# Kernel tuning notes

Hardware: AMD Instinct MI355X
Metric: run time of the kernel (lower is better)

## Reference

```python
import jax, jax.numpy as jnp
import numpy as np

OUT_H, OUT_W = 512, 512
BATCH, CHANNELS = 64, 3


def setup_inputs() -> dict:
    key = jax.random.key(0)
    k1, k2 = jax.random.split(key)
    U = jax.random.normal(k1, (BATCH, OUT_H, OUT_W, CHANNELS), dtype=jnp.float32)
    theta = jax.random.normal(k2, (BATCH, 1), dtype=jnp.float32)
    return {"U": U, "theta": theta}


def reference(U, theta):
    B = U.shape[0]
    H, W = OUT_H, OUT_W
    # normalized sampling grid [H*W, 3] with homogeneous coordinate
    gx, gy = jnp.meshgrid(jnp.linspace(-1.0, 1.0, W), jnp.linspace(-1.0, 1.0, H))
    grid = jnp.stack([gx, gy, jnp.ones_like(gx)], axis=-1).reshape(H * W, 3)
    # rotation-only affine matrix [B, 2, 3]
    cos_t, sin_t, z = jnp.cos(theta), jnp.sin(theta), jnp.zeros_like(theta)
    rot = jnp.concatenate([cos_t, -sin_t, z, sin_t, cos_t, z], axis=1).reshape(B, 2, 3)
    # transformed source coords [B, H*W, 2]
    T_g = jnp.einsum('bij,nj->bni', rot, grid)
    x = (T_g[..., 0] + 1.0) * (W - 1) / 2.0
    y = (T_g[..., 1] + 1.0) * (H - 1) / 2.0
    x0f = jnp.floor(x).astype(jnp.int32)
    y0f = jnp.floor(y).astype(jnp.int32)
    x0 = jnp.clip(x0f, 0, W - 1)
    x1 = jnp.clip(x0f + 1, 0, W - 1)
    y0 = jnp.clip(y0f, 0, H - 1)
    y1 = jnp.clip(y0f + 1, 0, H - 1)
    # 4-corner gathers, batched: [B, H*W, C]
    gather = jax.vmap(lambda u, yy, xx: u[yy, xx])
    Ia = gather(U, y0, x0)
    Ib = gather(U, y1, x0)
    Ic = gather(U, y0, x1)
    Id = gather(U, y1, x1)
    x0_f, x1_f = x0.astype(jnp.float32), x1.astype(jnp.float32)
    y0_f, y1_f = y0.astype(jnp.float32), y1.astype(jnp.float32)
    wa = (x1_f - x) * (y1_f - y)
    wb = (x1_f - x) * (y - y0_f)
    wc = (x - x0_f) * (y1_f - y)
    wd = (x - x0_f) * (y - y0_f)
    out = (wa[..., None] * Ia + wb[..., None] * Ib
           + wc[..., None] * Ic + wd[..., None] * Id)
    return out.reshape(B, H, W, -1)
```

## Files before the change

kernel.cpp:

```cpp
#include <hip/hip_runtime.h>
#include <hip/hip_fp16.h>

#define OUT_H 512
#define OUT_W 512
#define BATCH 64
#define CHANS 3

#define WROWS 48
#define WPX   48
#define RSTRIDE 98
#define LSZ 4704
#define IDXMAX (LSZ - 149)

struct Win {
    float xb0, yb0;
    int bx, by;
    bool interior;
};

__device__ __forceinline__ Win make_win(float xb0, float yb0, float c, float s) {
    float xmin = xb0 + fminf(0.0f, 31.0f * c) + fminf(0.0f, -31.0f * s);
    float ymin = yb0 + fminf(0.0f, 31.0f * s) + fminf(0.0f,  31.0f * c);
    float xmax = xb0 + fmaxf(0.0f, 31.0f * c) + fmaxf(0.0f, -31.0f * s);
    float ymax = yb0 + fmaxf(0.0f, 31.0f * s) + fmaxf(0.0f,  31.0f * c);
    Win w;
    int bx0 = min(max((int)floorf(xmin), 0), OUT_W - 1);
    int by0 = min(max((int)floorf(ymin), 0), OUT_H - 1);
    w.bx = min(bx0, OUT_W - WPX);
    w.by = min(by0, OUT_H - WROWS);
    w.interior = (xmin >= 0.0f) & (xmax < 510.0f) &
                 (ymin >= 0.0f) & (ymax < 510.0f);
    w.xb0 = xb0; w.yb0 = yb0;
    return w;
}

__device__ __forceinline__ void stage_load(const float* __restrict__ Ub,
                                           const Win& w, int tid, bool origin,
                                           float4 va[9]) {
    const float* gb = Ub + ((size_t)w.by * OUT_W + w.bx) * CHANS;
    if (!origin) {
#pragma unroll
        for (int k = 0; k < 9; ++k) {
            unsigned q = (unsigned)tid + 256u * k;
            unsigned r  = q / 48u;
            unsigned lx = q - r * 48u;
            va[k] = *(const float4*)(gb + (size_t)r * (OUT_W * CHANS) + lx * 3u - 1);
        }
    } else {
#pragma unroll
        for (int k = 0; k < 9; ++k) {
            unsigned q = (unsigned)tid + 256u * k;
            unsigned r  = q / 48u;
            unsigned lx = q - r * 48u;
            const float* p = gb + (size_t)r * (OUT_W * CHANS) + lx * 3u;
            float2 ab = *(const float2*)p;
            float  cc = p[2];
            va[k] = make_float4(0.0f, ab.x, ab.y, cc);
        }
    }
}

__device__ __forceinline__ void stage_write(unsigned int* smf, int tid,
                                            const float4 va[9]) {
#pragma unroll
    for (int k = 0; k < 9; ++k) {
        unsigned q = (unsigned)tid + 256u * k;
        unsigned r  = q / 48u;
        unsigned lx = q - r * 48u;
        unsigned slot = RSTRIDE * r + lx;
        float4 v = va[k];
        __half2 hA = __floats2half2_rn(v.y, v.z);
        __half2 hB = __floats2half2_rn(v.w, 0.0f);
        smf[slot]      = *(const unsigned int*)&hA;
        smf[slot + 49] = *(const unsigned int*)&hB;
    }
}

__device__ __forceinline__ void compute_store(const unsigned int* smf,
                                              const Win& w, float c, float s,
                                              int tid, float* __restrict__ po) {
    int il = tid >> 3;
    int jb = (tid & 7) << 2;
    float xr = w.xb0 + c * (float)jb - s * (float)il;
    float yr = w.yb0 + s * (float)jb + c * (float)il;
    int Koff = w.by * RSTRIDE + w.bx;
    bool interior = w.interior;

    float o[12];
#pragma unroll
    for (int p = 0; p < 4; ++p) {
        float x = fmaf(c, (float)p, xr);
        float y = fmaf(s, (float)p, yr);
        int ix = __float2int_rd(x);
        int iy = __float2int_rd(y);
        float fx = x - (float)ix;
        float fy = y - (float)iy;

        int idx = iy * RSTRIDE + ix - Koff;
        if (!interior) idx = min(max(idx, 0), IDXMAX);

        const unsigned int* lp = smf + idx;
        unsigned iA0 = lp[0],   iA1 = lp[1];
        unsigned iB0 = lp[49],  iB1 = lp[50];
        unsigned iA2 = lp[98],  iA3 = lp[99];
        unsigned iB2 = lp[147], iB3 = lp[148];

        __half2 fx2 = __float2half2_rn(fx);
        __half2 fy2 = __float2half2_rn(fy);
        __half2 a01 = *(const __half2*)&iA0, c01 = *(const __half2*)&iA1;
        __half2 a2  = *(const __half2*)&iB0, c2  = *(const __half2*)&iB1;
        __half2 b01 = *(const __half2*)&iA2, d01 = *(const __half2*)&iA3;
        __half2 b2  = *(const __half2*)&iB2, d2  = *(const __half2*)&iB3;

        __half2 t01 = __hfma2(fx2, __hsub2(c01, a01), a01);
        __half2 t2  = __hfma2(fx2, __hsub2(c2,  a2),  a2);
        __half2 u01 = __hfma2(fx2, __hsub2(d01, b01), b01);
        __half2 u2  = __hfma2(fx2, __hsub2(d2,  b2),  b2);
        __half2 r01 = __hfma2(fy2, __hsub2(u01, t01), t01);
        __half2 r2  = __hfma2(fy2, __hsub2(u2,  t2),  t2);

        float v0 = __low2float(r01);
        float v1 = __high2float(r01);
        float v2 = __low2float(r2);
        if (!interior) {
            bool valid = ((unsigned)ix < 511u) & ((unsigned)iy < 511u);
            v0 = valid ? v0 : 0.0f;
            v1 = valid ? v1 : 0.0f;
            v2 = valid ? v2 : 0.0f;
        }
        o[p * 3 + 0] = v0;
        o[p * 3 + 1] = v1;
        o[p * 3 + 2] = v2;
    }

    float* pr = po + (size_t)il * (OUT_W * CHANS) + jb * CHANS;
    ((float4*)pr)[0] = make_float4(o[0], o[1], o[2],  o[3]);
    ((float4*)pr)[1] = make_float4(o[4], o[5], o[6],  o[7]);
    ((float4*)pr)[2] = make_float4(o[8], o[9], o[10], o[11]);
}

__global__ __launch_bounds__(256) void st_bilinear_kernel(
    const float* __restrict__ U,
    const float* __restrict__ theta,
    float* __restrict__ out)
{
    __shared__ __align__(16) unsigned int smf[LSZ];

    int blk  = blockIdx.x;
    int lp   = (blk & 7) * 1024 + (blk >> 3);
    int b    = lp >> 7;
    int pair = lp & 127;
    int tr   = pair >> 3;
    int i0   = tr << 5;
    int j0A  = ((pair & 7) << 1) << 5;
    int tid  = threadIdx.x;

    float tt = theta[__builtin_amdgcn_readfirstlane(b)];
    float s, c;
    __sincosf(tt, &s, &c);

    const float scale = 2.0f / 511.0f;
    float gx0 = (float)j0A * scale - 1.0f;
    float gy0 = (float)i0  * scale - 1.0f;
    float xb0A = (c * gx0 - s * gy0 + 1.0f) * 255.5f;
    float yb0A = (s * gx0 + c * gy0 + 1.0f) * 255.5f;

    Win wA = make_win(xb0A, yb0A, c, s);
    Win wB = make_win(xb0A + 32.0f * c, yb0A + 32.0f * s, c, s);

    const float* Ub = U + (size_t)b * (OUT_H * OUT_W * CHANS);
    bool b0 = (b == 0);

    float4 va[9];
    stage_load(Ub, wA, tid, b0 & (wA.bx == 0) & (wA.by == 0), va);
    stage_write(smf, tid, va);

    float4 vb[9];
    stage_load(Ub, wB, tid, b0 & (wB.bx == 0) & (wB.by == 0), vb);

    __syncthreads();

    float* poA = out + (((size_t)b * OUT_H + i0) * OUT_W + j0A) * CHANS;
    compute_store(smf, wA, c, s, tid, poA);

    __syncthreads();

    stage_write(smf, tid, vb);

    __syncthreads();

    compute_store(smf, wB, c, s, tid, poA + 32 * CHANS);
}

extern "C" void kernel_launch(void* const* d_in, const int* in_sizes, int n_in,
                              void* d_out, int out_size, void* d_ws, size_t ws_size,
                              hipStream_t stream) {
    const float* U     = (const float*)d_in[0];
    const float* theta = (const float*)d_in[1];
    float* out = (float*)d_out;

    int blocks = BATCH * (OUT_H / 32) * (OUT_W / 32) / 2;
    st_bilinear_kernel<<<blocks, 256, 0, stream>>>(U, theta, out);
}
```

Measured before the change: 112.5 us.

## Process eight tiles per block with a software-pipelined load/compute loop

Each block now handles eight consecutive 32x32 tiles along a row instead of two, prefetching the next tile's window into registers while the current tile is computed from shared memory. The grid shrinks from 8192 to 2048 blocks, which amortizes per-block setup and overlaps global loads with compute across more tiles. The trade-off is fewer blocks in flight, which may lower occupancy-driven latency hiding and add barrier overhead per tile.

New measurement: 149.8 us. 1.33x slower.

```diff
diff --git a/kernel.cpp b/kernel.cpp
--- a/kernel.cpp
+++ b/kernel.cpp
@@ -147,12 +147,12 @@
     __shared__ __align__(16) unsigned int smf[LSZ];
 
     int blk  = blockIdx.x;
-    int lp   = (blk & 7) * 1024 + (blk >> 3);
-    int b    = lp >> 7;
-    int pair = lp & 127;
-    int tr   = pair >> 3;
-    int i0   = tr << 5;
-    int j0A  = ((pair & 7) << 1) << 5;
+    int lblk = (blk & 7) * 256 + (blk >> 3);
+    int base = lblk << 3;
+    int b    = base >> 8;
+    int rem  = base & 255;
+    int i0   = (rem >> 4) << 5;
+    int j0b  = (rem & 15) << 5;
     int tid  = threadIdx.x;
 
     float tt = theta[__builtin_amdgcn_readfirstlane(b)];
@@ -160,36 +160,34 @@
     __sincosf(tt, &s, &c);
 
     const float scale = 2.0f / 511.0f;
-    float gx0 = (float)j0A * scale - 1.0f;
+    float gx0 = (float)j0b * scale - 1.0f;
     float gy0 = (float)i0  * scale - 1.0f;
-    float xb0A = (c * gx0 - s * gy0 + 1.0f) * 255.5f;
-    float yb0A = (s * gx0 + c * gy0 + 1.0f) * 255.5f;
-
-    Win wA = make_win(xb0A, yb0A, c, s);
-    Win wB = make_win(xb0A + 32.0f * c, yb0A + 32.0f * s, c, s);
+    float xb = (c * gx0 - s * gy0 + 1.0f) * 255.5f;
+    float yb = (s * gx0 + c * gy0 + 1.0f) * 255.5f;
 
     const float* Ub = U + (size_t)b * (OUT_H * OUT_W * CHANS);
     bool b0 = (b == 0);
-
+    float* rowbase = out + (((size_t)b * OUT_H + i0) * OUT_W + j0b) * CHANS;
+
+    Win w = make_win(xb, yb, c, s);
     float4 va[9];
-    stage_load(Ub, wA, tid, b0 & (wA.bx == 0) & (wA.by == 0), va);
-    stage_write(smf, tid, va);
-
-    float4 vb[9];
-    stage_load(Ub, wB, tid, b0 & (wB.bx == 0) & (wB.by == 0), vb);
-
-    __syncthreads();
-
-    float* poA = out + (((size_t)b * OUT_H + i0) * OUT_W + j0A) * CHANS;
-    compute_store(smf, wA, c, s, tid, poA);
-
-    __syncthreads();
-
-    stage_write(smf, tid, vb);
-
-    __syncthreads();
-
-    compute_store(smf, wB, c, s, tid, poA + 32 * CHANS);
+    stage_load(Ub, w, tid, b0 & (w.bx == 0) & (w.by == 0), va);
+
+#pragma unroll 1
+    for (int t = 0; t < 8; ++t) {
+        stage_write(smf, tid, va);
+        Win wn = w;
+        if (t < 7) {
+            float xbn = xb + 32.0f * c * (float)(t + 1);
+            float ybn = yb + 32.0f * s * (float)(t + 1);
+            wn = make_win(xbn, ybn, c, s);
+            stage_load(Ub, wn, tid, b0 & (wn.bx == 0) & (wn.by == 0), va);
+        }
+        __syncthreads();
+        compute_store(smf, w, c, s, tid, rowbase + (size_t)(t << 5) * CHANS);
+        if (t < 7) __syncthreads();
+        w = wn;
+    }
 }
 
 extern "C" void kernel_launch(void* const* d_in, const int* in_sizes, int n_in,
@@ -199,6 +197,6 @@
     const float* theta = (const float*)d_in[1];
     float* out = (float*)d_out;
 
-    int blocks = BATCH * (OUT_H / 32) * (OUT_W / 32) / 2;
+    int blocks = 2048;
     st_bilinear_kernel<<<blocks, 256, 0, stream>>>(U, theta, out);
 }
```
